# Kernel tuning notes

Hardware: AMD Instinct MI355X
Metric: run time of the kernel (lower is better)

Reference implementation:

```python
import jax, jax.numpy as jnp
from jax import lax
import numpy as np

N3, N2, N1, N0 = 862, 1723, 3445, 6890  # mesh hierarchy (SMPL 6890 verts)
DEG, K = 16, 4  # nnz/row per Chebyshev support; K = order 3 + 1 supports


def _conv(x, w, b, s):
    y = lax.conv_general_dilated(x, w, (s, s), 'VALID', dimension_numbers=('NCHW', 'OIHW', 'NCHW'))
    return y + b[None, :, None, None]


def _pool(x):
    return lax.reduce_window(x, -jnp.inf, lax.max, (1, 1, 2, 2), (1, 1, 2, 2), 'VALID')


def _lin(x, w, b):
    return x @ w.T + b


def _rodrigues(r):  # [J,3] axis-angle -> [J,3,3] (batch_rodrigues)
    th = jnp.linalg.norm(r, axis=1, keepdims=True) + 1e-8
    k = r / th
    kx, ky, kz = k[:, 0], k[:, 1], k[:, 2]
    z = jnp.zeros_like(kx)
    Km = jnp.stack([z, -kz, ky, kz, z, -kx, -ky, kx, z], axis=1).reshape(-1, 3, 3)
    th = th[:, :, None]
    return jnp.eye(3, dtype=r.dtype)[None] + jnp.sin(th) * Km + (1.0 - jnp.cos(th)) * (Km @ Km)


def _spmm(idx, val, x):  # torch.sparse.mm with fixed nnz/row; idx,val: [N,D]
    return jnp.einsum('nd,ndf->nf', val, x[idx])


def _gcl(x, idx, val, W, b):  # Chebyshev graph conv: sum_k (A_k @ x) @ W_k + b
    return jnp.einsum('knd,kndf,kfo->no', val, x[idx], W) + b


def _basenet(frame, p):
    (c1w, c1b, c2w, c2b, c3w, c3b, c4w, c4b, c5w, c5b, fc1w, fc1b, fc4w, fc4b) = p
    c = _pool(jax.nn.relu(_conv(frame, c1w, c1b, 2)))
    c = _pool(jax.nn.relu(_conv(c, c2w, c2b, 1)))
    c = _pool(jax.nn.relu(_conv(c, c3w, c3b, 1)))
    c = _pool(jax.nn.relu(_conv(c, c4w, c4b, 1)))
    c = _pool(_conv(c, c5w, c5b, 1))  # [1,128,14,14]
    flat = jnp.transpose(c, (0, 3, 2, 1)).reshape(1, -1)  # torch.transpose(c,1,-1).reshape(1,-1)
    return _lin(flat, fc1w, fc1b), jax.nn.relu(_lin(flat, fc4w, fc4b))


def _forward(segmentations, poses, pose_mean, trans,
             c1w, c1b, c2w, c2b, c3w, c3b, c4w, c4b, c5w, c5b,
             fc1w, fc1b, fc2w, fc2b, fc3w, fc3b, fc4w, fc4b,
             fc5w, fc5b, fc6w, fc6b, fc7w, fc7b,
             gW3, gb3, gW2, gb2, gW1, gb1, gW0, gb0,
             av3, av2, av1, av0, uv2, uv1, uv0,
             ai3, ai2, ai1, ai0, ui2, ui1, ui0):
    nf = segmentations.shape[0]
    bp = (c1w, c1b, c2w, c2b, c3w, c3b, c4w, c4b, c5w, c5b, fc1w, fc1b, fc4w, fc4b)
    shape20, pose200 = jax.vmap(lambda f: _basenet(f, bp))(segmentations)  # [F,1,20],[F,1,200]
    pose_feat = jax.nn.relu(_lin(poses, fc5w, fc5b))  # [F,1,200]
    cat = jnp.concatenate([pose200, pose_feat], axis=-1)  # [F,1,400]
    pose_results = _lin(_lin(cat, fc6w, fc6b), fc7w, fc7b)  # [F,1,219]
    pm = pose_mean.at[:3].set(0.0)
    pose_init = _rodrigues(pm.reshape(-1, 3)).reshape(-1)  # [216]
    pct = jnp.concatenate([trans, pose_init])[None, None]  # [1,1,219]
    add = pose_results + pct
    add_poses = add[..., 3:].reshape(nf, -1, 24, 3, 3)
    add_trans = add[..., :3]
    betas_avr = shape20.reshape(-1, 20).mean(0)  # [20]
    betas_val = _lin(betas_avr, fc3w, fc3b)[None]  # [1,10]
    x = _lin(betas_avr, fc2w, fc2b).reshape(N3, 64)
    x = jax.nn.relu(_gcl(x, ai3, av3, gW3, gb3))  # [862,32]
    x = _spmm(ui2, uv2, x)                         # [1723,32]
    x = jax.nn.relu(_gcl(x, ai2, av2, gW2, gb2))  # [1723,16]
    x = _spmm(ui1, uv1, x)                         # [3445,16]
    x = jax.nn.relu(_gcl(x, ai1, av1, gW1, gb1))  # [3445,16]
    x = _spmm(ui0, uv0, x)                         # [6890,16]
    x = jnp.tanh(_gcl(x, ai0, av0, gW0, gb0))     # [6890,3]
    offsets = (x / 10.0)[None]
    return offsets, betas_val, add_poses, add_trans


def setup_inputs():
    ks = iter(jax.random.split(jax.random.key(0), 80))
    f32 = jnp.float32
    nrm = lambda shp, s: jax.random.normal(next(ks), shp, f32) * s
    uni = lambda shp, s: jax.random.uniform(next(ks), shp, f32) * s
    ri = lambda shp, hi: jax.random.randint(next(ks), shp, 0, hi)
    inp = {}
    inp['segmentations'] = nrm((8, 1, 3, 1017, 1017), 1.0)
    inp['poses'] = nrm((8, 1, 75), 1.0)
    inp['pose_mean'] = nrm((72,), 0.3)
    inp['trans'] = jnp.array([0.0, 0.2, -2.3], f32)
    for nm, shp, s in [('c1w', (8, 3, 3, 3), .1), ('c1b', (8,), .01), ('c2w', (16, 8, 3, 3), .1), ('c2b', (16,), .01),
                       ('c3w', (32, 16, 3, 3), .1), ('c3b', (32,), .01), ('c4w', (64, 32, 3, 3), .1), ('c4b', (64,), .01),
                       ('c5w', (128, 64, 3, 3), .1), ('c5b', (128,), .01),
                       ('fc1w', (20, 25088), .01), ('fc1b', (20,), .01), ('fc2w', (55168, 20), .05), ('fc2b', (55168,), .01),
                       ('fc3w', (10, 20), .05), ('fc3b', (10,), .01), ('fc4w', (200, 25088), .01), ('fc4b', (200,), .01),
                       ('fc5w', (200, 75), .05), ('fc5b', (200,), .01), ('fc6w', (100, 400), .05), ('fc6b', (100,), .01),
                       ('fc7w', (219, 100), .05), ('fc7b', (219,), .01),
                       ('gW3', (4, 64, 32), .1), ('gb3', (32,), .01), ('gW2', (4, 32, 16), .1), ('gb2', (16,), .01),
                       ('gW1', (4, 16, 16), .1), ('gb1', (16,), .01), ('gW0', (4, 16, 3), .1), ('gb0', (3,), .01)]:
        inp[nm] = nrm(shp, s)
    for nm, n in [('3', N3), ('2', N2), ('1', N1), ('0', N0)]:
        inp['av' + nm] = uni((K, n, DEG), 0.2)
        inp['ai' + nm] = ri((K, n, DEG), n)
    for nm, n_fine, n_coarse in [('2', N2, N3), ('1', N1, N2), ('0', N0, N1)]:
        inp['uv' + nm] = uni((n_fine, 4), 0.3)
        inp['ui' + nm] = ri((n_fine, 4), n_coarse)
    return inp


def reference(segmentations, poses, pose_mean, trans,
              c1w, c1b, c2w, c2b, c3w, c3b, c4w, c4b, c5w, c5b,
              fc1w, fc1b, fc2w, fc2b, fc3w, fc3b, fc4w, fc4b,
              fc5w, fc5b, fc6w, fc6b, fc7w, fc7b,
              gW3, gb3, gW2, gb2, gW1, gb1, gW0, gb0,
              av3, av2, av1, av0, uv2, uv1, uv0,
              ai3, ai2, ai1, ai0, ui2, ui1, ui0):
    return _forward(segmentations, poses, pose_mean, trans,
                    c1w, c1b, c2w, c2b, c3w, c3b, c4w, c4b, c5w, c5b,
                    fc1w, fc1b, fc2w, fc2b, fc3w, fc3b, fc4w, fc4b,
                    fc5w, fc5b, fc6w, fc6b, fc7w, fc7b,
                    gW3, gb3, gW2, gb2, gW1, gb1, gW0, gb0,
                    av3, av2, av1, av0, uv2, uv1, uv0,
                    ai3, ai2, ai1, ai0, ui2, ui1, ui0)
```

## Files before the change

### kernel.cpp

```cpp
#include <hip/hip_runtime.h>
#include <math.h>

__global__ __launch_bounds__(256) void conv1_lds(
    const float* __restrict__ in, const float* __restrict__ w,
    const float* __restrict__ bias, float* __restrict__ out)
{
    constexpr int Hin = 1017, P = 254;
    __shared__ float li[17][4][65];
    const int f  = blockIdx.y;
    const int ct = blockIdx.x & 3;
    const int rt = blockIdx.x >> 2;
    const int t  = threadIdx.x;
    const int lane = t & 63, wid = t >> 6;
    const int row0 = rt * 16, col0 = ct * 256;
    const float* inf = in + (size_t)f * 3 * Hin * Hin;

    const int ph = rt * 4 + wid, pw = ct * 64 + lane;
    const bool wactive = (ph < P) && (pw < P);

    float acc[32];
    #pragma unroll
    for (int i = 0; i < 32; i++) acc[i] = 0.f;

    for (int ic = 0; ic < 3; ic++) {
        __syncthreads();
        const float* src = inf + (size_t)ic * Hin * Hin;
        #pragma unroll
        for (int i = 0; i < 17; i++) {
            int gr = row0 + i; if (gr > Hin - 1) gr = Hin - 1;
            int gc = col0 + t; if (gc > Hin - 1) gc = Hin - 1;
            li[i][t & 3][t >> 2] = src[(size_t)gr * Hin + gc];
        }
        if (t < 17) {
            int gr = row0 + t; if (gr > Hin - 1) gr = Hin - 1;
            int gc = col0 + 256; if (gc > Hin - 1) gc = Hin - 1;
            li[t][0][64] = src[(size_t)gr * Hin + gc];
        }
        __syncthreads();

        float win[25];
        #pragma unroll
        for (int r = 0; r < 5; r++)
            #pragma unroll
            for (int c = 0; c < 5; c++)
                win[r * 5 + c] = li[4 * wid + r][c & 3][lane + (c >> 2)];

        #pragma unroll
        for (int oc = 0; oc < 8; oc++) {
            float wr[9];
            #pragma unroll
            for (int j = 0; j < 9; j++) wr[j] = w[(oc * 3 + ic) * 9 + j];
            #pragma unroll
            for (int py = 0; py < 2; py++)
                #pragma unroll
                for (int px = 0; px < 2; px++) {
                    float s = acc[(oc * 2 + py) * 2 + px];
                    #pragma unroll
                    for (int kh = 0; kh < 3; kh++)
                        #pragma unroll
                        for (int kw = 0; kw < 3; kw++)
                            s += wr[kh * 3 + kw] * win[(2 * py + kh) * 5 + (2 * px + kw)];
                    acc[(oc * 2 + py) * 2 + px] = s;
                }
        }
    }

    if (wactive) {
        #pragma unroll
        for (int oc = 0; oc < 8; oc++) {
            float m = fmaxf(fmaxf(acc[oc * 4 + 0], acc[oc * 4 + 1]),
                            fmaxf(acc[oc * 4 + 2], acc[oc * 4 + 3]));
            m = fmaxf(m + bias[oc], 0.f);
            out[(((size_t)f * 8 + oc) * P + ph) * P + pw] = m;
        }
    }
}

template<int IC, int OCG, bool RELU, bool FLATOUT>
__global__ __launch_bounds__(256) void conv_pool_s1(
    const float* __restrict__ in, const float* __restrict__ w,
    const float* __restrict__ bias, float* __restrict__ out,
    int Hin, int P, int OC)
{
    const int f = blockIdx.y, g = blockIdx.z;
    int tid = blockIdx.x * 256 + threadIdx.x;
    if (tid >= P * P) return;
    int ph = tid / P, pw = tid % P;
    const float* inf = in + ((size_t)f * IC) * Hin * Hin + (size_t)(2 * ph) * Hin + 2 * pw;
    const float* wg = w + (size_t)g * OCG * IC * 9;

    float acc[OCG * 4];
    #pragma unroll
    for (int i = 0; i < OCG * 4; i++) acc[i] = 0.f;

    for (int ic = 0; ic < IC; ic++) {
        const float* p = inf + (size_t)ic * Hin * Hin;
        float win[4][4];
        #pragma unroll
        for (int r = 0; r < 4; r++) {
            float2 a = *(const float2*)(p + (size_t)r * Hin);
            float2 b = *(const float2*)(p + (size_t)r * Hin + 2);
            win[r][0] = a.x; win[r][1] = a.y; win[r][2] = b.x; win[r][3] = b.y;
        }
        #pragma unroll
        for (int oc = 0; oc < OCG; oc++) {
            float wr[9];
            #pragma unroll
            for (int j = 0; j < 9; j++) wr[j] = wg[(oc * IC + ic) * 9 + j];
            #pragma unroll
            for (int py = 0; py < 2; py++)
                #pragma unroll
                for (int px = 0; px < 2; px++) {
                    float s = acc[(oc * 2 + py) * 2 + px];
                    #pragma unroll
                    for (int kh = 0; kh < 3; kh++)
                        #pragma unroll
                        for (int kw = 0; kw < 3; kw++)
                            s += wr[kh * 3 + kw] * win[py + kh][px + kw];
                    acc[(oc * 2 + py) * 2 + px] = s;
                }
        }
    }

    #pragma unroll
    for (int oc = 0; oc < OCG; oc++) {
        float m = fmaxf(fmaxf(acc[oc * 4 + 0], acc[oc * 4 + 1]),
                        fmaxf(acc[oc * 4 + 2], acc[oc * 4 + 3]));
        m += bias[g * OCG + oc];
        if (RELU) m = fmaxf(m, 0.f);
        int ocg = g * OCG + oc;
        if (FLATOUT) {
            out[(size_t)f * (P * P * OC) + (pw * P + ph) * OC + ocg] = m;
        } else {
            out[(((size_t)f * OC + ocg) * P + ph) * P + pw] = m;
        }
    }
}

__global__ __launch_bounds__(256) void fc_head(
    const float* __restrict__ flat,
    const float* __restrict__ fc1w, const float* __restrict__ fc1b,
    const float* __restrict__ fc4w, const float* __restrict__ fc4b,
    float* __restrict__ shape20, float* __restrict__ pose200)
{
    int o = blockIdx.x;
    const float* W = (o < 20) ? fc1w + (size_t)o * 25088
                              : fc4w + (size_t)(o - 20) * 25088;
    const float4* W4  = (const float4*)W;
    const float4* fl4 = (const float4*)flat;
    float acc[8];
    #pragma unroll
    for (int f = 0; f < 8; f++) acc[f] = 0.f;
    for (int i = threadIdx.x; i < 6272; i += 256) {
        float4 wv = W4[i];
        #pragma unroll
        for (int f = 0; f < 8; f++) {
            float4 xv = fl4[f * 6272 + i];
            acc[f] += wv.x * xv.x + wv.y * xv.y + wv.z * xv.z + wv.w * xv.w;
        }
    }
    #pragma unroll
    for (int f = 0; f < 8; f++)
        for (int off = 32; off > 0; off >>= 1)
            acc[f] += __shfl_down(acc[f], off, 64);
    __shared__ float red[4][8];
    int wid = threadIdx.x >> 6, lane = threadIdx.x & 63;
    if (lane == 0) {
        #pragma unroll
        for (int f = 0; f < 8; f++) red[wid][f] = acc[f];
    }
    __syncthreads();
    if (threadIdx.x < 8) {
        int f = threadIdx.x;
        float s = red[0][f] + red[1][f] + red[2][f] + red[3][f];
        if (o < 20) shape20[f * 20 + o] = s + fc1b[o];
        else        pose200[f * 200 + (o - 20)] = fmaxf(s + fc4b[o - 20], 0.f);
    }
}

__global__ __launch_bounds__(256) void pose_fc5(
    const float* __restrict__ poses,
    const float* __restrict__ fc5w, const float* __restrict__ fc5b,
    float* __restrict__ pose_feat)
{
    int t = blockIdx.x * 256 + threadIdx.x;
    if (t >= 8 * 200) return;
    int f = t / 200, o = t % 200;
    float s = fc5b[o];
    const float* pr = poses + f * 75;
    const float* wr = fc5w + o * 75;
    #pragma unroll 5
    for (int j = 0; j < 75; j++) s += pr[j] * wr[j];
    pose_feat[f * 200 + o] = fmaxf(s, 0.f);
}

__global__ __launch_bounds__(256) void pose_fc6(
    const float* __restrict__ pose200, const float* __restrict__ pose_feat,
    const float* __restrict__ fc6w, const float* __restrict__ fc6b,
    float* __restrict__ t1)
{
    int wv = blockIdx.x * 4 + (threadIdx.x >> 6);
    int lane = threadIdx.x & 63;
    if (wv >= 8 * 100) return;
    int f = wv / 100, o = wv % 100;
    float s = 0.f;
    for (int j = lane; j < 400; j += 64) {
        float xv = (j < 200) ? pose200[f * 200 + j] : pose_feat[f * 200 + (j - 200)];
        s += xv * fc6w[o * 400 + j];
    }
    #pragma unroll
    for (int off = 32; off > 0; off >>= 1) s += __shfl_down(s, off, 64);
    if (lane == 0) t1[f * 100 + o] = s + fc6b[o];
}

__global__ __launch_bounds__(256) void pose_fc7(
    const float* __restrict__ t1, const float* __restrict__ fc7w,
    const float* __restrict__ fc7b, const float* __restrict__ pose_mean,
    const float* __restrict__ trans, float* __restrict__ out)
{
    int wv = blockIdx.x * 4 + (threadIdx.x >> 6);
    int lane = threadIdx.x & 63;
    if (wv >= 8 * 219) return;
    int f = wv / 219, c = wv % 219;
    float s = 0.f;
    {
        float xv = t1[f * 100 + lane];
        s += xv * fc7w[c * 100 + lane];
        int j2 = lane + 64;
        if (j2 < 100) s += t1[f * 100 + j2] * fc7w[c * 100 + j2];
    }
    #pragma unroll
    for (int off = 32; off > 0; off >>= 1) s += __shfl_down(s, off, 64);
    if (lane != 0) return;
    s += fc7b[c];
    float pct;
    if (c < 3) {
        pct = trans[c];
    } else {
        int j = (c - 3) / 9, e = (c - 3) % 9;
        float rx = (j == 0) ? 0.f : pose_mean[3 * j + 0];
        float ry = (j == 0) ? 0.f : pose_mean[3 * j + 1];
        float rz = (j == 0) ? 0.f : pose_mean[3 * j + 2];
        float th = sqrtf(rx * rx + ry * ry + rz * rz) + 1e-8f;
        float kx = rx / th, ky = ry / th, kz = rz / th;
        float sn = sinf(th), c2 = 1.f - cosf(th);
        float R[9];
        R[0] = 1.f - c2 * (ky * ky + kz * kz);
        R[1] = -sn * kz + c2 * (kx * ky);
        R[2] =  sn * ky + c2 * (kx * kz);
        R[3] =  sn * kz + c2 * (kx * ky);
        R[4] = 1.f - c2 * (kx * kx + kz * kz);
        R[5] = -sn * kx + c2 * (ky * kz);
        R[6] = -sn * ky + c2 * (kx * kz);
        R[7] =  sn * kx + c2 * (ky * kz);
        R[8] = 1.f - c2 * (kx * kx + ky * ky);
        pct = R[e];
    }
    s += pct;
    if (c < 3) out[22408 + f * 3 + c] = s;
    else       out[20680 + f * 216 + (c - 3)] = s;
}

__global__ __launch_bounds__(256) void betas_fc2(
    const float* __restrict__ shape20,
    const float* __restrict__ fc2w, const float* __restrict__ fc2b,
    const float* __restrict__ fc3w, const float* __restrict__ fc3b,
    float* __restrict__ x0, float* __restrict__ out)
{
    __shared__ float avr[20];
    int t = threadIdx.x;
    if (t < 20) {
        float s = 0.f;
        for (int f = 0; f < 8; f++) s += shape20[f * 20 + t];
        avr[t] = s * 0.125f;
    }
    __syncthreads();
    int r = blockIdx.x * 256 + t;
    if (r < 55168) {
        float s = fc2b[r];
        #pragma unroll
        for (int j = 0; j < 20; j++) s += fc2w[(size_t)r * 20 + j] * avr[j];
        x0[r] = s;
    }
    if (blockIdx.x == 0 && t < 10) {
        float s = fc3b[t];
        for (int j = 0; j < 20; j++) s += fc3w[t * 20 + j] * avr[j];
        out[20670 + t] = s;
    }
}

template<int F, int O, int ACT>
__global__ __launch_bounds__(256) void gcl(
    const float* __restrict__ x, const int* __restrict__ ai,
    const float* __restrict__ av, const float* __restrict__ gW,
    const float* __restrict__ gb, float* __restrict__ y, int N)
{
    constexpr int VPW = 64 / F;
    constexpr int VPB = 4 * VPW;
    constexpr int HS  = 4 * F + 8;
    __shared__ float h[VPB][HS];

    int wid = threadIdx.x >> 6, lane = threadIdx.x & 63;
    {
        int vl = wid * VPW + (VPW == 1 ? 0 : lane / F);
        int fl = lane % F;
        int n = blockIdx.x * VPB + vl;
        if (n < N) {
            #pragma unroll
            for (int k = 0; k < 4; k++) {
                const int*   ip = ai + ((size_t)k * N + n) * 16;
                const float* vp = av + ((size_t)k * N + n) * 16;
                float s = 0.f;
                #pragma unroll
                for (int d = 0; d < 16; d++)
                    s += vp[d] * x[(size_t)ip[d] * F + fl];
                h[vl][k * F + fl] = s;
            }
        }
    }
    __syncthreads();

    int t = threadIdx.x;
    if (t < VPB * O) {
        int vl = t / O, o = t % O;
        int n = blockIdx.x * VPB + vl;
        if (n < N) {
            float s = gb[o];
            #pragma unroll
            for (int k = 0; k < 4; k++)
                for (int f2 = 0; f2 < F; f2++)
                    s += h[vl][k * F + f2] * gW[((size_t)k * F + f2) * O + o];
            if (ACT == 0) s = fmaxf(s, 0.f);
            else          s = tanhf(s) * 0.1f;
            y[(size_t)n * O + o] = s;
        }
    }
}

template<int F>
__global__ __launch_bounds__(256) void spmm(
    const float* __restrict__ x, const int* __restrict__ ui,
    const float* __restrict__ uv, float* __restrict__ y, int N)
{
    int t = blockIdx.x * 256 + threadIdx.x;
    if (t >= N * F) return;
    int n = t / F, f = t % F;
    float s = 0.f;
    #pragma unroll
    for (int j = 0; j < 4; j++)
        s += uv[n * 4 + j] * x[(size_t)ui[n * 4 + j] * F + f];
    y[t] = s;
}

extern "C" void kernel_launch(void* const* d_in, const int* in_sizes, int n_in,
                              void* d_out, int out_size, void* d_ws, size_t ws_size,
                              hipStream_t stream) {
    (void)in_sizes; (void)n_in; (void)out_size; (void)ws_size;

    const float* seg   = (const float*)d_in[0];
    const float* poses = (const float*)d_in[1];
    const float* pmean = (const float*)d_in[2];
    const float* trans = (const float*)d_in[3];
    const float* c1w = (const float*)d_in[4];  const float* c1b = (const float*)d_in[5];
    const float* c2w = (const float*)d_in[6];  const float* c2b = (const float*)d_in[7];
    const float* c3w = (const float*)d_in[8];  const float* c3b = (const float*)d_in[9];
    const float* c4w = (const float*)d_in[10]; const float* c4b = (const float*)d_in[11];
    const float* c5w = (const float*)d_in[12]; const float* c5b = (const float*)d_in[13];
    const float* fc1w = (const float*)d_in[14]; const float* fc1b = (const float*)d_in[15];
    const float* fc2w = (const float*)d_in[16]; const float* fc2b = (const float*)d_in[17];
    const float* fc3w = (const float*)d_in[18]; const float* fc3b = (const float*)d_in[19];
    const float* fc4w = (const float*)d_in[20]; const float* fc4b = (const float*)d_in[21];
    const float* fc5w = (const float*)d_in[22]; const float* fc5b = (const float*)d_in[23];
    const float* fc6w = (const float*)d_in[24]; const float* fc6b = (const float*)d_in[25];
    const float* fc7w = (const float*)d_in[26]; const float* fc7b = (const float*)d_in[27];
    const float* gW3 = (const float*)d_in[28]; const float* gb3 = (const float*)d_in[29];
    const float* gW2 = (const float*)d_in[30]; const float* gb2 = (const float*)d_in[31];
    const float* gW1 = (const float*)d_in[32]; const float* gb1 = (const float*)d_in[33];
    const float* gW0 = (const float*)d_in[34]; const float* gb0 = (const float*)d_in[35];
    const float* av3 = (const float*)d_in[36]; const int* ai3 = (const int*)d_in[37];
    const float* av2 = (const float*)d_in[38]; const int* ai2 = (const int*)d_in[39];
    const float* av1 = (const float*)d_in[40]; const int* ai1 = (const int*)d_in[41];
    const float* av0 = (const float*)d_in[42]; const int* ai0 = (const int*)d_in[43];
    const float* uv2 = (const float*)d_in[44]; const int* ui2 = (const int*)d_in[45];
    const float* uv1 = (const float*)d_in[46]; const int* ui1 = (const int*)d_in[47];
    const float* uv0 = (const float*)d_in[48]; const int* ui0 = (const int*)d_in[49];

    float* W = (float*)d_ws;
    float* out = (float*)d_out;

    float* pool1 = W + 0;
    float* pool2 = W + 4129024;
    float* pool3 = W + 0;
    float* pool4 = W + 4129024;
    float* flat5 = W + 4589824;
    float* shape20 = W + 1000000;
    float* pose200 = shape20 + 160;
    float* x0  = pose200 + 1600;
    float* y3  = x0 + 55168;
    float* x2  = y3 + 27584;
    float* y2  = x2 + 55136;
    float* x1  = y2 + 27568;
    float* y1  = x1 + 55120;
    float* x0u = y1 + 55120;
    float* pose_feat = x0u + 110240;
    float* t1 = pose_feat + 1600;

    conv1_lds<<<dim3(256, 8), 256, 0, stream>>>(seg, c1w, c1b, pool1);
    conv_pool_s1<8, 16, true, false>
        <<<dim3(63, 8, 1), 256, 0, stream>>>(pool1, c2w, c2b, pool2, 254, 126, 16);
    conv_pool_s1<16, 16, true, false>
        <<<dim3(16, 8, 2), 256, 0, stream>>>(pool2, c3w, c3b, pool3, 126, 62, 32);
    conv_pool_s1<32, 8, true, false>
        <<<dim3(4, 8, 8), 256, 0, stream>>>(pool3, c4w, c4b, pool4, 62, 30, 64);
    conv_pool_s1<64, 2, false, true>
        <<<dim3(1, 8, 64), 256, 0, stream>>>(pool4, c5w, c5b, flat5, 30, 14, 128);

    fc_head<<<dim3(220), 256, 0, stream>>>(flat5, fc1w, fc1b, fc4w, fc4b, shape20, pose200);
    pose_fc5<<<dim3(7),   256, 0, stream>>>(poses, fc5w, fc5b, pose_feat);
    pose_fc6<<<dim3(200), 256, 0, stream>>>(pose200, pose_feat, fc6w, fc6b, t1);
    pose_fc7<<<dim3(438), 256, 0, stream>>>(t1, fc7w, fc7b, pmean, trans, out);
    betas_fc2<<<dim3(216), 256, 0, stream>>>(shape20, fc2w, fc2b, fc3w, fc3b, x0, out);

    gcl<64, 32, 0><<<dim3(216),  256, 0, stream>>>(x0,  ai3, av3, gW3, gb3, y3, 862);
    spmm<32>      <<<dim3(216),  256, 0, stream>>>(y3,  ui2, uv2, x2, 1723);
    gcl<32, 16, 0><<<dim3(216),  256, 0, stream>>>(x2,  ai2, av2, gW2, gb2, y2, 1723);
    spmm<16>      <<<dim3(216),  256, 0, stream>>>(y2,  ui1, uv1, x1, 3445);
    gcl<16, 16, 0><<<dim3(216),  256, 0, stream>>>(x1,  ai1, av1, gW1, gb1, y1, 3445);
    spmm<16>      <<<dim3(431),  256, 0, stream>>>(y1,  ui0, uv0, x0u, 6890);
    gcl<16, 3, 1> <<<dim3(431),  256, 0, stream>>>(x0u, ai0, av0, gW0, gb0, out, 6890);
}
```

Before: 192.6 us.

## Fuse pose MLP into one kernel, fold upsampling into GCL, retile convs

Merges the three pose FC kernels into one block-per-frame kernel that keeps its intermediates in shared memory. Folds each upsampling spmm into the following graph-conv gather, recomputing the 4-tap interpolation on the fly for every neighbor access. Also halves the output-channel tile of conv2–conv4 and doubles their z-grid for more blocks. This removes several launches and intermediate buffers, but the gather work in the upsampled GCLs grows roughly fourfold and the pose kernel runs on only 8 blocks.

Measured after the change: 279.8 us. 1.45x slower.

```diff
diff --git a/kernel.cpp b/kernel.cpp
--- a/kernel.cpp
+++ b/kernel.cpp
@@ -178,87 +178,74 @@
     }
 }
 
-__global__ __launch_bounds__(256) void pose_fc5(
-    const float* __restrict__ poses,
+__global__ __launch_bounds__(256) void pose_all(
+    const float* __restrict__ poses, const float* __restrict__ pose_mean,
+    const float* __restrict__ trans,
     const float* __restrict__ fc5w, const float* __restrict__ fc5b,
-    float* __restrict__ pose_feat)
-{
-    int t = blockIdx.x * 256 + threadIdx.x;
-    if (t >= 8 * 200) return;
-    int f = t / 200, o = t % 200;
-    float s = fc5b[o];
-    const float* pr = poses + f * 75;
-    const float* wr = fc5w + o * 75;
-    #pragma unroll 5
-    for (int j = 0; j < 75; j++) s += pr[j] * wr[j];
-    pose_feat[f * 200 + o] = fmaxf(s, 0.f);
-}
-
-__global__ __launch_bounds__(256) void pose_fc6(
-    const float* __restrict__ pose200, const float* __restrict__ pose_feat,
     const float* __restrict__ fc6w, const float* __restrict__ fc6b,
-    float* __restrict__ t1)
-{
-    int wv = blockIdx.x * 4 + (threadIdx.x >> 6);
-    int lane = threadIdx.x & 63;
-    if (wv >= 8 * 100) return;
-    int f = wv / 100, o = wv % 100;
-    float s = 0.f;
-    for (int j = lane; j < 400; j += 64) {
-        float xv = (j < 200) ? pose200[f * 200 + j] : pose_feat[f * 200 + (j - 200)];
-        s += xv * fc6w[o * 400 + j];
-    }
-    #pragma unroll
-    for (int off = 32; off > 0; off >>= 1) s += __shfl_down(s, off, 64);
-    if (lane == 0) t1[f * 100 + o] = s + fc6b[o];
-}
-
-__global__ __launch_bounds__(256) void pose_fc7(
-    const float* __restrict__ t1, const float* __restrict__ fc7w,
-    const float* __restrict__ fc7b, const float* __restrict__ pose_mean,
-    const float* __restrict__ trans, float* __restrict__ out)
-{
-    int wv = blockIdx.x * 4 + (threadIdx.x >> 6);
-    int lane = threadIdx.x & 63;
-    if (wv >= 8 * 219) return;
-    int f = wv / 219, c = wv % 219;
-    float s = 0.f;
-    {
-        float xv = t1[f * 100 + lane];
-        s += xv * fc7w[c * 100 + lane];
-        int j2 = lane + 64;
-        if (j2 < 100) s += t1[f * 100 + j2] * fc7w[c * 100 + j2];
-    }
-    #pragma unroll
-    for (int off = 32; off > 0; off >>= 1) s += __shfl_down(s, off, 64);
-    if (lane != 0) return;
-    s += fc7b[c];
-    float pct;
-    if (c < 3) {
-        pct = trans[c];
-    } else {
-        int j = (c - 3) / 9, e = (c - 3) % 9;
-        float rx = (j == 0) ? 0.f : pose_mean[3 * j + 0];
-        float ry = (j == 0) ? 0.f : pose_mean[3 * j + 1];
-        float rz = (j == 0) ? 0.f : pose_mean[3 * j + 2];
-        float th = sqrtf(rx * rx + ry * ry + rz * rz) + 1e-8f;
-        float kx = rx / th, ky = ry / th, kz = rz / th;
-        float sn = sinf(th), c2 = 1.f - cosf(th);
-        float R[9];
-        R[0] = 1.f - c2 * (ky * ky + kz * kz);
-        R[1] = -sn * kz + c2 * (kx * ky);
-        R[2] =  sn * ky + c2 * (kx * kz);
-        R[3] =  sn * kz + c2 * (kx * ky);
-        R[4] = 1.f - c2 * (kx * kx + kz * kz);
-        R[5] = -sn * kx + c2 * (ky * kz);
-        R[6] = -sn * ky + c2 * (kx * kz);
-        R[7] =  sn * kx + c2 * (ky * kz);
-        R[8] = 1.f - c2 * (kx * kx + ky * ky);
-        pct = R[e];
-    }
-    s += pct;
-    if (c < 3) out[22408 + f * 3 + c] = s;
-    else       out[20680 + f * 216 + (c - 3)] = s;
+    const float* __restrict__ fc7w, const float* __restrict__ fc7b,
+    const float* __restrict__ pose200, float* __restrict__ out)
+{
+    __shared__ float cat[400];
+    __shared__ float t1s[100];
+    __shared__ float pl[75];
+    const int f = blockIdx.x, t = threadIdx.x;
+    if (t < 75) pl[t] = poses[f * 75 + t];
+    __syncthreads();
+
+    for (int c = t; c < 400; c += 256) {
+        float v;
+        if (c < 200) {
+            v = pose200[f * 200 + c];
+        } else {
+            int o = c - 200;
+            float s = fc5b[o];
+            #pragma unroll 5
+            for (int j = 0; j < 75; j++) s += pl[j] * fc5w[o * 75 + j];
+            v = fmaxf(s, 0.f);
+        }
+        cat[c] = v;
+    }
+    __syncthreads();
+
+    if (t < 100) {
+        float s = fc6b[t];
+        for (int j = 0; j < 400; j++) s += cat[j] * fc6w[t * 400 + j];
+        t1s[t] = s;
+    }
+    __syncthreads();
+
+    if (t < 219) {
+        const int c = t;
+        float s = fc7b[c];
+        for (int j = 0; j < 100; j++) s += t1s[j] * fc7w[c * 100 + j];
+        float pct;
+        if (c < 3) {
+            pct = trans[c];
+        } else {
+            int j = (c - 3) / 9, e = (c - 3) % 9;
+            float rx = (j == 0) ? 0.f : pose_mean[3 * j + 0];
+            float ry = (j == 0) ? 0.f : pose_mean[3 * j + 1];
+            float rz = (j == 0) ? 0.f : pose_mean[3 * j + 2];
+            float th = sqrtf(rx * rx + ry * ry + rz * rz) + 1e-8f;
+            float kx = rx / th, ky = ry / th, kz = rz / th;
+            float sn = sinf(th), c2 = 1.f - cosf(th);
+            float R[9];
+            R[0] = 1.f - c2 * (ky * ky + kz * kz);
+            R[1] = -sn * kz + c2 * (kx * ky);
+            R[2] =  sn * ky + c2 * (kx * kz);
+            R[3] =  sn * kz + c2 * (kx * ky);
+            R[4] = 1.f - c2 * (kx * kx + kz * kz);
+            R[5] = -sn * kx + c2 * (ky * kz);
+            R[6] = -sn * ky + c2 * (kx * kz);
+            R[7] =  sn * kx + c2 * (ky * kz);
+            R[8] = 1.f - c2 * (kx * kx + ky * ky);
+            pct = R[e];
+        }
+        s += pct;
+        if (c < 3) out[22408 + f * 3 + c] = s;
+        else       out[20680 + f * 216 + (c - 3)] = s;
+    }
 }
 
 __global__ __launch_bounds__(256) void betas_fc2(
@@ -289,9 +276,10 @@
     }
 }
 
-template<int F, int O, int ACT>
+template<int F, int O, int ACT, int UP>
 __global__ __launch_bounds__(256) void gcl(
-    const float* __restrict__ x, const int* __restrict__ ai,
+    const float* __restrict__ x, const int* __restrict__ ui,
+    const float* __restrict__ uv, const int* __restrict__ ai,
     const float* __restrict__ av, const float* __restrict__ gW,
     const float* __restrict__ gb, float* __restrict__ y, int N)
 {
@@ -312,8 +300,21 @@
                 const float* vp = av + ((size_t)k * N + n) * 16;
                 float s = 0.f;
                 #pragma unroll
-                for (int d = 0; d < 16; d++)
-                    s += vp[d] * x[(size_t)ip[d] * F + fl];
+                for (int d = 0; d < 16; d++) {
+                    int m = ip[d];
+                    float xv;
+                    if (UP) {
+                        const int*   up = ui + (size_t)m * 4;
+                        const float* wp = uv + (size_t)m * 4;
+                        xv = wp[0] * x[(size_t)up[0] * F + fl]
+                           + wp[1] * x[(size_t)up[1] * F + fl]
+                           + wp[2] * x[(size_t)up[2] * F + fl]
+                           + wp[3] * x[(size_t)up[3] * F + fl];
+                    } else {
+                        xv = x[(size_t)m * F + fl];
+                    }
+                    s += vp[d] * xv;
+                }
                 h[vl][k * F + fl] = s;
             }
         }
@@ -335,21 +336,6 @@
             y[(size_t)n * O + o] = s;
         }
     }
-}
-
-template<int F>
-__global__ __launch_bounds__(256) void spmm(
-    const float* __restrict__ x, const int* __restrict__ ui,
-    const float* __restrict__ uv, float* __restrict__ y, int N)
-{
-    int t = blockIdx.x * 256 + threadIdx.x;
-    if (t >= N * F) return;
-    int n = t / F, f = t % F;
-    float s = 0.f;
-    #pragma unroll
-    for (int j = 0; j < 4; j++)
-        s += uv[n * 4 + j] * x[(size_t)ui[n * 4 + j] * F + f];
-    y[t] = s;
 }
 
 extern "C" void kernel_launch(void* const* d_in, const int* in_sizes, int n_in,
@@ -397,35 +383,26 @@
     float* pose200 = shape20 + 160;
     float* x0  = pose200 + 1600;
     float* y3  = x0 + 55168;
-    float* x2  = y3 + 27584;
-    float* y2  = x2 + 55136;
-    float* x1  = y2 + 27568;
-    float* y1  = x1 + 55120;
-    float* x0u = y1 + 55120;
-    float* pose_feat = x0u + 110240;
-    float* t1 = pose_feat + 1600;
+    float* y2  = y3 + 27584;
+    float* y1  = y2 + 27568;
 
     conv1_lds<<<dim3(256, 8), 256, 0, stream>>>(seg, c1w, c1b, pool1);
-    conv_pool_s1<8, 16, true, false>
-        <<<dim3(63, 8, 1), 256, 0, stream>>>(pool1, c2w, c2b, pool2, 254, 126, 16);
-    conv_pool_s1<16, 16, true, false>
-        <<<dim3(16, 8, 2), 256, 0, stream>>>(pool2, c3w, c3b, pool3, 126, 62, 32);
-    conv_pool_s1<32, 8, true, false>
-        <<<dim3(4, 8, 8), 256, 0, stream>>>(pool3, c4w, c4b, pool4, 62, 30, 64);
+    conv_pool_s1<8, 8, true, false>
+        <<<dim3(63, 8, 2), 256, 0, stream>>>(pool1, c2w, c2b, pool2, 254, 126, 16);
+    conv_pool_s1<16, 8, true, false>
+        <<<dim3(16, 8, 4), 256, 0, stream>>>(pool2, c3w, c3b, pool3, 126, 62, 32);
+    conv_pool_s1<32, 4, true, false>
+        <<<dim3(4, 8, 16), 256, 0, stream>>>(pool3, c4w, c4b, pool4, 62, 30, 64);
     conv_pool_s1<64, 2, false, true>
         <<<dim3(1, 8, 64), 256, 0, stream>>>(pool4, c5w, c5b, flat5, 30, 14, 128);
 
     fc_head<<<dim3(220), 256, 0, stream>>>(flat5, fc1w, fc1b, fc4w, fc4b, shape20, pose200);
-    pose_fc5<<<dim3(7),   256, 0, stream>>>(poses, fc5w, fc5b, pose_feat);
-    pose_fc6<<<dim3(200), 256, 0, stream>>>(pose200, pose_feat, fc6w, fc6b, t1);
-    pose_fc7<<<dim3(438), 256, 0, stream>>>(t1, fc7w, fc7b, pmean, trans, out);
+    pose_all<<<dim3(8), 256, 0, stream>>>(poses, pmean, trans, fc5w, fc5b, fc6w, fc6b,
+                                          fc7w, fc7b, pose200, out);
     betas_fc2<<<dim3(216), 256, 0, stream>>>(shape20, fc2w, fc2b, fc3w, fc3b, x0, out);
 
-    gcl<64, 32, 0><<<dim3(216),  256, 0, stream>>>(x0,  ai3, av3, gW3, gb3, y3, 862);
-    spmm<32>      <<<dim3(216),  256, 0, stream>>>(y3,  ui2, uv2, x2, 1723);
-    gcl<32, 16, 0><<<dim3(216),  256, 0, stream>>>(x2,  ai2, av2, gW2, gb2, y2, 1723);
-    spmm<16>      <<<dim3(216),  256, 0, stream>>>(y2,  ui1, uv1, x1, 3445);
-    gcl<16, 16, 0><<<dim3(216),  256, 0, stream>>>(x1,  ai1, av1, gW1, gb1, y1, 3445);
-    spmm<16>      <<<dim3(431),  256, 0, stream>>>(y1,  ui0, uv0, x0u, 6890);
-    gcl<16, 3, 1> <<<dim3(431),  256, 0, stream>>>(x0u, ai0, av0, gW0, gb0, out, 6890);
-}
+    gcl<64, 32, 0, 0><<<dim3(216), 256, 0, stream>>>(x0, nullptr, nullptr, ai3, av3, gW3, gb3, y3, 862);
+    gcl<32, 16, 0, 1><<<dim3(216), 256, 0, stream>>>(y3, ui2, uv2, ai2, av2, gW2, gb2, y2, 1723);
+    gcl<16, 16, 0, 1><<<dim3(216), 256, 0, stream>>>(y2, ui1, uv1, ai1, av1, gW1, gb1, y1, 3445);
+    gcl<16, 3, 1, 1> <<<dim3(431), 256, 0, stream>>>(y1, ui0, uv0, ai0, av0, gW0, gb0, out, 6890);
+}
```
